# Kernel optimization log

Measured on AMD Instinct MI355X. Metric: run time of the kernel, lower is better.

## Reference

```python
import jax, jax.numpy as jnp
import numpy as np

N_HEAD = 8
EPS = 1e-6  # LayerNorm2d eps


def setup_inputs() -> dict:
    key = jax.random.key(0)
    ks = jax.random.split(key, 7)
    B, C, H, W = 16, 256, 128, 128
    nh, dk, dv = N_HEAD, 32, 32
    s = 1.0 / np.sqrt(C)
    return {
        "q": jax.random.normal(ks[0], (B, C, H, W), jnp.float32),
        "k": jax.random.normal(ks[1], (B, C, H, W), jnp.float32),
        "v": jax.random.normal(ks[2], (B, C, H, W), jnp.float32),
        # 1x1 convs without bias == channel matmuls; weight shape [out_ch, in_ch]
        "wq": jax.random.normal(ks[3], (nh * dk, C), jnp.float32) * s,
        "wk": jax.random.normal(ks[4], (nh * dk, C), jnp.float32) * s,
        "wv": jax.random.normal(ks[5], (nh * dv, C), jnp.float32) * s,
        "wfc": jax.random.normal(ks[6], (C, nh * dv), jnp.float32) * (1.0 / np.sqrt(nh * dv)),
        "ln_w": jnp.ones((C,), jnp.float32),
        "ln_b": jnp.zeros((C,), jnp.float32),
        "kernel": 5,
        "pad": 2,
    }


def _forward(q, k, v, wq, wk, wv, wfc, ln_w, ln_b, kernel, pad):
    B, C, H, W = q.shape
    nh = N_HEAD
    dk = wq.shape[0] // nh
    dv = wv.shape[0] // nh
    assert kernel == 2 * pad + 1
    residual = q
    # 1x1 conv projections, split into heads: [B, nh, d, H, W]
    qh = jnp.einsum('oc,bchw->bohw', wq, q).reshape(B, nh, dk, H, W)
    kh = jnp.einsum('oc,bchw->bohw', wk, k).reshape(B, nh, dk, H, W)
    vh = jnp.einsum('oc,bchw->bohw', wv, v).reshape(B, nh, dv, H, W)
    # zero-pad spatially: out-of-bounds correlations/values are zero, matching the
    # original bilinear sampler (zeros padding) and the custom padding() helper.
    kp = jnp.pad(kh, ((0, 0), (0, 0), (0, 0), (pad, pad), (pad, pad)))
    vp = jnp.pad(vh, ((0, 0), (0, 0), (0, 0), (pad, pad), (pad, pad)))
    # local correlation volume: dot(q[i,j], k[i+dy-pad, j+dx-pad]) for the KxK window
    # (integer offsets -> bilinear sample degenerates to a gather). Never materializes
    # the full [B, HW, HW] matrix the torch code builds before sampling.
    corr = jnp.stack(
        [jnp.einsum('bncij,bncij->bnij', qh, kp[:, :, :, dy:dy + H, dx:dx + W])
         for dy in range(kernel) for dx in range(kernel)], axis=-1)  # [B,nh,H,W,K*K]
    # relu (from CorrBlock.corr), temperature = sqrt(d_k), softmax over window.
    # OOB entries are 0 (not -inf), faithfully matching the original.
    attn = jax.nn.softmax(jax.nn.relu(corr) / jnp.float32(np.sqrt(dk)), axis=-1)
    # channel attention: per-pixel weighted sum of v over the same window
    out = jnp.zeros((B, nh, dv, H, W), q.dtype)
    idx = 0
    for dy in range(kernel):
        for dx in range(kernel):
            out = out + attn[:, :, :, :, idx][:, :, None] * vp[:, :, :, dy:dy + H, dx:dx + W]
            idx += 1
    o = jnp.einsum('oc,bchw->bohw', wfc, out.reshape(B, nh * dv, H, W)) + residual
    # LayerNorm2d: normalize over channel dim per pixel
    mu = o.mean(1, keepdims=True)
    var = ((o - mu) ** 2).mean(1, keepdims=True)
    y = (o - mu) / jnp.sqrt(var + EPS)
    return ln_w[None, :, None, None] * y + ln_b[None, :, None, None]


def reference(q, k, v, wq, wk, wv, wfc, ln_w, ln_b, kernel, pad):
    return _forward(q, k, v, wq, wk, wv, wfc, ln_w, ln_b, kernel, pad)
```

## Files before the change

kernel.cpp:

```cpp
#include <hip/hip_runtime.h>
#include <hip/hip_bf16.h>

#define BATCH 16
#define CH 256
#define HH 128
#define WW 128
#define HWSZ (HH * WW)
#define NHEAD 8
#define DHEAD 32
#define PW 132
#define PPIX (132 * 132)
#define ROWS 264

typedef __attribute__((ext_vector_type(8))) short bf16x8;
typedef __attribute__((ext_vector_type(4))) float f32x4;
typedef _Float16 h2v __attribute__((ext_vector_type(2)));

__device__ __forceinline__ unsigned short f2h(float f) {
    _Float16 h = (_Float16)f;
    return __builtin_bit_cast(unsigned short, h);
}
__device__ __forceinline__ unsigned pkbf(float a, float b) {
    __hip_bfloat162_raw r = __hip_bfloat162_raw(__float22bfloat162_rn(make_float2(a, b)));
    return (unsigned)r.x | ((unsigned)r.y << 16);
}

#if __has_builtin(__builtin_amdgcn_fdot2)
#define DOT2(a, b, c) __builtin_amdgcn_fdot2((a), (b), (c), false)
#else
#define DOT2(a, b, c) ((c) + (float)(a)[0] * (float)(b)[0] + (float)(a)[1] * (float)(b)[1])
#endif

__global__ __launch_bounds__(256)
void zpad_kernel(unsigned short* __restrict__ kpad, unsigned short* __restrict__ vpad)
{
    int bid = blockIdx.x;
    unsigned short* dst = ((bid & 1) ? vpad : kpad) + (size_t)(bid >> 1) * PPIX * DHEAD;
    const uint4 z = {0u, 0u, 0u, 0u};
    for (int i = threadIdx.x; i < 1040; i += 256) {
        int row, col;
        if (i < 264)      { row = i / 132; col = i - row * 132; }
        else if (i < 528) { int j = i - 264; int r = j / 132; row = 130 + r; col = j - r * 132; }
        else              { int j = i - 528; row = 2 + (j >> 2); int c = j & 3; col = (c < 2) ? c : (128 + c); }
        uint4* p = reinterpret_cast<uint4*>(dst + (size_t)(row * PW + col) * DHEAD);
        p[0] = z; p[1] = z; p[2] = z; p[3] = z;
    }
}

__global__ __launch_bounds__(256)
void prep_kernel(const float* __restrict__ wq, const float* __restrict__ wk,
                 const float* __restrict__ wv, const float* __restrict__ wfc,
                 unsigned short* __restrict__ wb)
{
    const float* src = (blockIdx.y == 0) ? wq : (blockIdx.y == 1) ? wk
                     : (blockIdx.y == 2) ? wv : wfc;
    unsigned short* dst = wb + blockIdx.y * 65536;
    int e = (blockIdx.x * 256 + threadIdx.x) * 8;
    const float4* s = reinterpret_cast<const float4*>(src + e);
    float4 a = s[0], c = s[1];
    uint4 u;
    u.x = pkbf(a.x, a.y); u.y = pkbf(a.z, a.w);
    u.z = pkbf(c.x, c.y); u.w = pkbf(c.z, c.w);
    *reinterpret_cast<uint4*>(dst + e) = u;
}

__global__ __launch_bounds__(512)
void proj_kernel(const float* __restrict__ q, const float* __restrict__ k,
                 const float* __restrict__ v, const unsigned short* __restrict__ wb,
                 unsigned short* __restrict__ qh, unsigned short* __restrict__ kpad,
                 unsigned short* __restrict__ vpad)
{
    __shared__ __align__(16) unsigned short lB[64 * ROWS];

    const int t = threadIdx.x;
    const int b = blockIdx.y;
    const int p0 = blockIdx.x * 64;
    const int z = blockIdx.z;

    const float* X; unsigned short* Y;
    if (z == 0)      { X = q; Y = qh; }
    else if (z == 1) { X = k; Y = kpad; }
    else             { X = v; Y = vpad; }
    const unsigned short* Wb = wb + z * 65536;
    X += (size_t)b * CH * HWSZ;
    const size_t pixstride = (z == 0) ? (size_t)HWSZ : (size_t)PPIX;
    Y += (size_t)b * NHEAD * pixstride * DHEAD;

    const int lane = t & 63;
    const int wid  = t >> 6;
    const int lrow = lane & 15;
    const int lkg  = lane >> 4;
    const int pB   = t & 63;
    const int cg   = t >> 6;
    const int psw  = pB >> 3;

    float fv[32];
    {
        const float* xb = X + p0 + pB + (size_t)(cg * 32) * HWSZ;
#pragma unroll
        for (int i = 0; i < 32; ++i) fv[i] = xb[(size_t)i * HWSZ];
    }
    __builtin_amdgcn_sched_barrier(0);
#pragma unroll
    for (int i = 0; i < 4; ++i) {
        uint4 u;
        u.x = pkbf(fv[i*8+0], fv[i*8+1]); u.y = pkbf(fv[i*8+2], fv[i*8+3]);
        u.z = pkbf(fv[i*8+4], fv[i*8+5]); u.w = pkbf(fv[i*8+6], fv[i*8+7]);
        *reinterpret_cast<uint4*>(&lB[pB * ROWS + ((cg * 4 + i) ^ psw) * 8]) = u;
    }

    bf16x8 afc[2], afn[2];
#pragma unroll
    for (int m = 0; m < 2; ++m)
        afc[m] = *reinterpret_cast<const bf16x8*>(Wb + (wid * 32 + m * 16 + lrow) * 256 + lkg * 8);

    f32x4 acc[2][4];
    const f32x4 zero = {0.f, 0.f, 0.f, 0.f};
#pragma unroll
    for (int m = 0; m < 2; ++m)
#pragma unroll
        for (int n = 0; n < 4; ++n) acc[m][n] = zero;

    __syncthreads();

#pragma unroll
    for (int ks = 0; ks < 8; ++ks) {
        if (ks < 7) {
#pragma unroll
            for (int m = 0; m < 2; ++m)
                afn[m] = *reinterpret_cast<const bf16x8*>(Wb + (wid * 32 + m * 16 + lrow) * 256 + (ks + 1) * 32 + lkg * 8);
        }
        bf16x8 bfv[4];
#pragma unroll
        for (int n = 0; n < 4; ++n) {
            int row = n * 16 + lrow;
            bfv[n] = *reinterpret_cast<const bf16x8*>(&lB[row * ROWS + ((ks * 4 + lkg) ^ (row >> 3)) * 8]);
        }
#pragma unroll
        for (int m = 0; m < 2; ++m)
#pragma unroll
            for (int n = 0; n < 4; ++n)
                acc[m][n] = __builtin_amdgcn_mfma_f32_16x16x32_bf16(afc[m], bfv[n], acc[m][n], 0, 0, 0);
#pragma unroll
        for (int m = 0; m < 2; ++m) afc[m] = afn[m];
    }

    const int lr = lane >> 4, lc = lane & 15;
#pragma unroll
    for (int m = 0; m < 2; ++m)
#pragma unroll
        for (int n = 0; n < 4; ++n) {
            int d0 = m * 16 + lr * 4;
            int p = p0 + n * 16 + lc;
            ushort4 pk;
            pk.x = f2h(acc[m][n][0]); pk.y = f2h(acc[m][n][1]);
            pk.z = f2h(acc[m][n][2]); pk.w = f2h(acc[m][n][3]);
            size_t pix;
            if (z == 0) pix = (size_t)wid * HWSZ + p;
            else { int row = p >> 7, col = p & 127; pix = (size_t)wid * PPIX + (size_t)(row + 2) * PW + (col + 2); }
            *reinterpret_cast<ushort4*>(&Y[pix * DHEAD + d0]) = pk;
        }
}

__global__ __launch_bounds__(1024)
void attn_kernel(unsigned short* __restrict__ qh,
                 const unsigned short* __restrict__ kpad,
                 const unsigned short* __restrict__ vpad)
{
    const int t = threadIdx.x;
    const int swz = (blockIdx.x & 7) * 1024 + (blockIdx.x >> 3);
    const int bh = swz >> 6;
    const int tile = swz & 63;
    const int x0 = (tile & 7) * 16, y0 = (tile >> 3) * 16;
    const int qc = t & 3;
    const int px = (t >> 2) & 15;
    const int py = t >> 6;
    const int gx = x0 + px, gy = y0 + py;

    unsigned short* qp = qh + ((size_t)bh * HWSZ + gy * WW + gx) * DHEAD + qc * 8;
    const unsigned short* kb = kpad + (size_t)bh * PPIX * DHEAD + qc * 8;
    const unsigned short* vb = vpad + (size_t)bh * PPIX * DHEAD + qc * 8;

    union { uint4 u; h2v h2[4]; } Q;
    Q.u = *reinterpret_cast<const uint4*>(qp);

    float ew[25];
#pragma unroll
    for (int wy = 0; wy < 5; ++wy) {
        const unsigned short* krow = kb + (size_t)((gy + wy) * PW + gx) * DHEAD;
#pragma unroll
        for (int wx = 0; wx < 5; ++wx) {
            union { uint4 u; h2v h2[4]; } K;
            K.u = *reinterpret_cast<const uint4*>(krow + wx * DHEAD);
            float s = 0.f;
#pragma unroll
            for (int j = 0; j < 4; ++j)
                s = DOT2(Q.h2[j], K.h2[j], s);
            s += __shfl_xor(s, 1);
            s += __shfl_xor(s, 2);
            ew[wy * 5 + wx] = __expf(fmaxf(s, 0.f) * 0.17677669529663687f);
        }
    }

    float sum = 0.f;
#pragma unroll
    for (int i = 0; i < 25; ++i) sum += ew[i];
    const float inv = 1.f / sum;

    union { uint4 u; h2v h2[4]; } A;
    const h2v hz = {(_Float16)0.f, (_Float16)0.f};
#pragma unroll
    for (int j = 0; j < 4; ++j) A.h2[j] = hz;

#pragma unroll
    for (int wy = 0; wy < 5; ++wy) {
        const unsigned short* vrow = vb + (size_t)((gy + wy) * PW + gx) * DHEAD;
#pragma unroll
        for (int wx = 0; wx < 5; ++wx) {
            _Float16 wh = (_Float16)(ew[wy * 5 + wx] * inv);
            h2v w2 = {wh, wh};
            union { uint4 u; h2v h2[4]; } V;
            V.u = *reinterpret_cast<const uint4*>(vrow + wx * DHEAD);
#pragma unroll
            for (int j = 0; j < 4; ++j)
                A.h2[j] += w2 * V.h2[j];
        }
    }

    uint4 o;
    o.x = pkbf((float)A.h2[0][0], (float)A.h2[0][1]);
    o.y = pkbf((float)A.h2[1][0], (float)A.h2[1][1]);
    o.z = pkbf((float)A.h2[2][0], (float)A.h2[2][1]);
    o.w = pkbf((float)A.h2[3][0], (float)A.h2[3][1]);
    *reinterpret_cast<uint4*>(qp) = o;
}

__global__ __launch_bounds__(512)
void fcln_kernel(const unsigned short* __restrict__ ob, const unsigned short* __restrict__ wfcb,
                 const float* __restrict__ qres, const float* __restrict__ lnw,
                 const float* __restrict__ lnb, float* __restrict__ out)
{
    __shared__ __align__(16) unsigned short lB[64 * ROWS];
    __shared__ float lsum[8][64];
    __shared__ float lssq[8][64];

    const int t = threadIdx.x;
    const int b = blockIdx.y;
    const int p0 = blockIdx.x * 64;

    const int lane = t & 63;
    const int wid  = t >> 6;
    const int lrow = lane & 15;
    const int lkg  = lane >> 4;

    uint4 bv[4];
#pragma unroll
    for (int r = 0; r < 4; ++r) {
        int idx = r * 512 + t;
        int h  = idx >> 8;
        int rem = idx & 255;
        int px = rem >> 2, qc = rem & 3;
        bv[r] = *reinterpret_cast<const uint4*>(
            ob + ((size_t)(b * NHEAD + h) * HWSZ + p0 + px) * DHEAD + qc * 8);
    }
    __builtin_amdgcn_sched_barrier(0);
#pragma unroll
    for (int r = 0; r < 4; ++r) {
        int idx = r * 512 + t;
        int h  = idx >> 8;
        int rem = idx & 255;
        int px = rem >> 2, qc = rem & 3;
        *reinterpret_cast<uint4*>(&lB[px * ROWS + ((h * 4 + qc) ^ (px >> 3)) * 8]) = bv[r];
    }

    bf16x8 afc[2], afn[2];
#pragma unroll
    for (int m = 0; m < 2; ++m)
        afc[m] = *reinterpret_cast<const bf16x8*>(wfcb + (wid * 32 + m * 16 + lrow) * 256 + lkg * 8);

    f32x4 acc[2][4];
    const f32x4 zero = {0.f, 0.f, 0.f, 0.f};
#pragma unroll
    for (int m = 0; m < 2; ++m)
#pragma unroll
        for (int n = 0; n < 4; ++n) acc[m][n] = zero;

    __syncthreads();

#pragma unroll
    for (int ks = 0; ks < 8; ++ks) {
        if (ks < 7) {
#pragma unroll
            for (int m = 0; m < 2; ++m)
                afn[m] = *reinterpret_cast<const bf16x8*>(wfcb + (wid * 32 + m * 16 + lrow) * 256 + (ks + 1) * 32 + lkg * 8);
        }
        bf16x8 bfv[4];
#pragma unroll
        for (int n = 0; n < 4; ++n) {
            int row = n * 16 + lrow;
            bfv[n] = *reinterpret_cast<const bf16x8*>(&lB[row * ROWS + ((ks * 4 + lkg) ^ (row >> 3)) * 8]);
        }
#pragma unroll
        for (int m = 0; m < 2; ++m)
#pragma unroll
            for (int n = 0; n < 4; ++n)
                acc[m][n] = __builtin_amdgcn_mfma_f32_16x16x32_bf16(afc[m], bfv[n], acc[m][n], 0, 0, 0);
#pragma unroll
        for (int m = 0; m < 2; ++m) afc[m] = afn[m];
    }

    const int lr = lane >> 4, lc = lane & 15;
    const float* qb = qres + (size_t)b * CH * HWSZ;
#pragma unroll
    for (int m = 0; m < 2; ++m)
#pragma unroll
        for (int n = 0; n < 4; ++n)
#pragma unroll
            for (int j = 0; j < 4; ++j) {
                int o = wid * 32 + m * 16 + lr * 4 + j;
                int p = p0 + n * 16 + lc;
                acc[m][n][j] += qb[(size_t)o * HWSZ + p];
            }

    float s[4], s2[4];
#pragma unroll
    for (int n = 0; n < 4; ++n) {
        float a = 0.f, c2 = 0.f;
#pragma unroll
        for (int m = 0; m < 2; ++m)
#pragma unroll
            for (int j = 0; j < 4; ++j) {
                float x = acc[m][n][j];
                a += x; c2 += x * x;
            }
        a  += __shfl_xor(a, 16);  a  += __shfl_xor(a, 32);
        c2 += __shfl_xor(c2, 16); c2 += __shfl_xor(c2, 32);
        s[n] = a; s2[n] = c2;
    }
    if (lane < 16) {
#pragma unroll
        for (int n = 0; n < 4; ++n) {
            lsum[wid][n * 16 + lane] = s[n];
            lssq[wid][n * 16 + lane] = s2[n];
        }
    }
    __syncthreads();

    float mu[4], rs[4];
#pragma unroll
    for (int n = 0; n < 4; ++n) {
        int p = n * 16 + lc;
        float ts = 0.f, tq = 0.f;
#pragma unroll
        for (int w = 0; w < 8; ++w) { ts += lsum[w][p]; tq += lssq[w][p]; }
        float m_ = ts * (1.f / 256.f);
        float v_ = tq * (1.f / 256.f) - m_ * m_;
        mu[n] = m_;
        rs[n] = rsqrtf(v_ + 1e-6f);
    }

    float* op = out + (size_t)b * CH * HWSZ;
#pragma unroll
    for (int m = 0; m < 2; ++m)
#pragma unroll
        for (int j = 0; j < 4; ++j) {
            int o = wid * 32 + m * 16 + lr * 4 + j;
            float g = lnw[o], bb = lnb[o];
#pragma unroll
            for (int n = 0; n < 4; ++n) {
                int p = p0 + n * 16 + lc;
                op[(size_t)o * HWSZ + p] = (acc[m][n][j] - mu[n]) * rs[n] * g + bb;
            }
        }
}

extern "C" void kernel_launch(void* const* d_in, const int* in_sizes, int n_in,
                              void* d_out, int out_size, void* d_ws, size_t ws_size,
                              hipStream_t stream) {
    const float* q   = (const float*)d_in[0];
    const float* k   = (const float*)d_in[1];
    const float* v   = (const float*)d_in[2];
    const float* wq  = (const float*)d_in[3];
    const float* wk  = (const float*)d_in[4];
    const float* wv  = (const float*)d_in[5];
    const float* wfc = (const float*)d_in[6];
    const float* lnw = (const float*)d_in[7];
    const float* lnb = (const float*)d_in[8];

    const size_t qsz = (size_t)BATCH * NHEAD * HWSZ * DHEAD;
    const size_t psz = (size_t)BATCH * NHEAD * PPIX * DHEAD;
    if (ws_size < (qsz + 2 * psz + 4 * 65536) * sizeof(unsigned short)) return;

    unsigned short* qh = (unsigned short*)d_ws;
    unsigned short* kp = qh + qsz;
    unsigned short* vp = kp + psz;
    unsigned short* wb = vp + psz;

    zpad_kernel<<<256, 256, 0, stream>>>(kp, vp);
    prep_kernel<<<dim3(32, 4), 256, 0, stream>>>(wq, wk, wv, wfc, wb);
    proj_kernel<<<dim3(HWSZ / 64, BATCH, 3), 512, 0, stream>>>(q, k, v, wb, qh, kp, vp);
    attn_kernel<<<8192, 1024, 0, stream>>>(qh, kp, vp);
    fcln_kernel<<<dim3(HWSZ / 64, BATCH), 512, 0, stream>>>(qh, wb + 3 * 65536, q, lnw, lnb, (float*)d_out);
}
```

Baseline: 783.7 us.

## Make projection and fc+LN kernels persistent with double-buffered LDS prefetch

The projection and fc+layernorm kernels now launch a fixed grid of 512 persistent blocks, each looping over several 64-pixel tiles (24 for projection, 8 for fc). The next tile's global loads are issued before the current tile's MFMA work and packed into a second LDS buffer afterward, overlapping memory latency with compute. The aim is to cut block launch overhead and hide load latency. In exchange, fv registers stay live across the loop, LDS use doubles, and parallelism is bounded by 512 blocks.

```diff
diff --git a/kernel.cpp b/kernel.cpp
--- a/kernel.cpp
+++ b/kernel.cpp
@@ -11,6 +11,9 @@
 #define PW 132
 #define PPIX (132 * 132)
 #define ROWS 264
+#define NBLK 512
+#define NITP 24
+#define NITF 8
 
 typedef __attribute__((ext_vector_type(8))) short bf16x8;
 typedef __attribute__((ext_vector_type(4))) float f32x4;
@@ -64,28 +67,15 @@
     *reinterpret_cast<uint4*>(dst + e) = u;
 }
 
-__global__ __launch_bounds__(512)
+__global__ __launch_bounds__(512, 4)
 void proj_kernel(const float* __restrict__ q, const float* __restrict__ k,
                  const float* __restrict__ v, const unsigned short* __restrict__ wb,
                  unsigned short* __restrict__ qh, unsigned short* __restrict__ kpad,
                  unsigned short* __restrict__ vpad)
 {
-    __shared__ __align__(16) unsigned short lB[64 * ROWS];
+    __shared__ __align__(16) unsigned short lB[2][64 * ROWS];
 
     const int t = threadIdx.x;
-    const int b = blockIdx.y;
-    const int p0 = blockIdx.x * 64;
-    const int z = blockIdx.z;
-
-    const float* X; unsigned short* Y;
-    if (z == 0)      { X = q; Y = qh; }
-    else if (z == 1) { X = k; Y = kpad; }
-    else             { X = v; Y = vpad; }
-    const unsigned short* Wb = wb + z * 65536;
-    X += (size_t)b * CH * HWSZ;
-    const size_t pixstride = (z == 0) ? (size_t)HWSZ : (size_t)PPIX;
-    Y += (size_t)b * NHEAD * pixstride * DHEAD;
-
     const int lane = t & 63;
     const int wid  = t >> 6;
     const int lrow = lane & 15;
@@ -94,72 +84,103 @@
     const int cg   = t >> 6;
     const int psw  = pB >> 3;
 
+    const int gbase = blockIdx.x * NITP;
+
+    auto xptr = [&](int g) -> const float* {
+        int z = g >> 12, b = (g >> 8) & 15;
+        const float* X = (z == 0) ? q : (z == 1) ? k : v;
+        return X + (size_t)b * CH * HWSZ + (g & 255) * 64;
+    };
+
     float fv[32];
     {
-        const float* xb = X + p0 + pB + (size_t)(cg * 32) * HWSZ;
+        const float* xb = xptr(gbase) + pB + (size_t)(cg * 32) * HWSZ;
 #pragma unroll
         for (int i = 0; i < 32; ++i) fv[i] = xb[(size_t)i * HWSZ];
     }
-    __builtin_amdgcn_sched_barrier(0);
 #pragma unroll
     for (int i = 0; i < 4; ++i) {
         uint4 u;
         u.x = pkbf(fv[i*8+0], fv[i*8+1]); u.y = pkbf(fv[i*8+2], fv[i*8+3]);
         u.z = pkbf(fv[i*8+4], fv[i*8+5]); u.w = pkbf(fv[i*8+6], fv[i*8+7]);
-        *reinterpret_cast<uint4*>(&lB[pB * ROWS + ((cg * 4 + i) ^ psw) * 8]) = u;
-    }
-
-    bf16x8 afc[2], afn[2];
-#pragma unroll
-    for (int m = 0; m < 2; ++m)
-        afc[m] = *reinterpret_cast<const bf16x8*>(Wb + (wid * 32 + m * 16 + lrow) * 256 + lkg * 8);
-
-    f32x4 acc[2][4];
-    const f32x4 zero = {0.f, 0.f, 0.f, 0.f};
-#pragma unroll
-    for (int m = 0; m < 2; ++m)
-#pragma unroll
-        for (int n = 0; n < 4; ++n) acc[m][n] = zero;
-
+        *reinterpret_cast<uint4*>(&lB[0][pB * ROWS + ((cg * 4 + i) ^ psw) * 8]) = u;
+    }
     __syncthreads();
 
-#pragma unroll
-    for (int ks = 0; ks < 8; ++ks) {
-        if (ks < 7) {
-#pragma unroll
-            for (int m = 0; m < 2; ++m)
-                afn[m] = *reinterpret_cast<const bf16x8*>(Wb + (wid * 32 + m * 16 + lrow) * 256 + (ks + 1) * 32 + lkg * 8);
-        }
-        bf16x8 bfv[4];
-#pragma unroll
-        for (int n = 0; n < 4; ++n) {
-            int row = n * 16 + lrow;
-            bfv[n] = *reinterpret_cast<const bf16x8*>(&lB[row * ROWS + ((ks * 4 + lkg) ^ (row >> 3)) * 8]);
-        }
+    for (int it = 0; it < NITP; ++it) {
+        const int g = gbase + it;
+        const int z = g >> 12;
+        const int b = (g >> 8) & 15;
+        const int p0 = (g & 255) * 64;
+
+        if (it + 1 < NITP) {
+            const float* xb = xptr(g + 1) + pB + (size_t)(cg * 32) * HWSZ;
+#pragma unroll
+            for (int i = 0; i < 32; ++i) fv[i] = xb[(size_t)i * HWSZ];
+        }
+
+        const unsigned short* Wb = wb + z * 65536;
+        f32x4 acc[2][4];
+        const f32x4 zero = {0.f, 0.f, 0.f, 0.f};
 #pragma unroll
         for (int m = 0; m < 2; ++m)
 #pragma unroll
-            for (int n = 0; n < 4; ++n)
-                acc[m][n] = __builtin_amdgcn_mfma_f32_16x16x32_bf16(afc[m], bfv[n], acc[m][n], 0, 0, 0);
-#pragma unroll
-        for (int m = 0; m < 2; ++m) afc[m] = afn[m];
-    }
-
-    const int lr = lane >> 4, lc = lane & 15;
-#pragma unroll
-    for (int m = 0; m < 2; ++m)
-#pragma unroll
-        for (int n = 0; n < 4; ++n) {
-            int d0 = m * 16 + lr * 4;
-            int p = p0 + n * 16 + lc;
-            ushort4 pk;
-            pk.x = f2h(acc[m][n][0]); pk.y = f2h(acc[m][n][1]);
-            pk.z = f2h(acc[m][n][2]); pk.w = f2h(acc[m][n][3]);
-            size_t pix;
-            if (z == 0) pix = (size_t)wid * HWSZ + p;
-            else { int row = p >> 7, col = p & 127; pix = (size_t)wid * PPIX + (size_t)(row + 2) * PW + (col + 2); }
-            *reinterpret_cast<ushort4*>(&Y[pix * DHEAD + d0]) = pk;
-        }
+            for (int n = 0; n < 4; ++n) acc[m][n] = zero;
+
+#pragma unroll
+        for (int ks = 0; ks < 8; ++ks) {
+            bf16x8 af[2];
+#pragma unroll
+            for (int m = 0; m < 2; ++m)
+                af[m] = *reinterpret_cast<const bf16x8*>(Wb + (wid * 32 + m * 16 + lrow) * 256 + ks * 32 + lkg * 8);
+            bf16x8 bfv[4];
+#pragma unroll
+            for (int n = 0; n < 4; ++n) {
+                int row = n * 16 + lrow;
+                bfv[n] = *reinterpret_cast<const bf16x8*>(&lB[it & 1][row * ROWS + ((ks * 4 + lkg) ^ (row >> 3)) * 8]);
+            }
+#pragma unroll
+            for (int m = 0; m < 2; ++m)
+#pragma unroll
+                for (int n = 0; n < 4; ++n)
+                    acc[m][n] = __builtin_amdgcn_mfma_f32_16x16x32_bf16(af[m], bfv[n], acc[m][n], 0, 0, 0);
+        }
+
+        {
+            unsigned short* Y;
+            size_t pixstride;
+            if (z == 0)      { Y = qh;   pixstride = HWSZ; }
+            else if (z == 1) { Y = kpad; pixstride = PPIX; }
+            else             { Y = vpad; pixstride = PPIX; }
+            Y += (size_t)b * NHEAD * pixstride * DHEAD;
+            const int lr = lane >> 4, lc = lane & 15;
+#pragma unroll
+            for (int m = 0; m < 2; ++m)
+#pragma unroll
+                for (int n = 0; n < 4; ++n) {
+                    int d0 = m * 16 + lr * 4;
+                    int p = p0 + n * 16 + lc;
+                    ushort4 pk;
+                    pk.x = f2h(acc[m][n][0]); pk.y = f2h(acc[m][n][1]);
+                    pk.z = f2h(acc[m][n][2]); pk.w = f2h(acc[m][n][3]);
+                    size_t pix;
+                    if (z == 0) pix = (size_t)wid * HWSZ + p;
+                    else { int row = p >> 7, col = p & 127; pix = (size_t)wid * PPIX + (size_t)(row + 2) * PW + (col + 2); }
+                    *reinterpret_cast<ushort4*>(&Y[pix * DHEAD + d0]) = pk;
+                }
+        }
+
+        if (it + 1 < NITP) {
+#pragma unroll
+            for (int i = 0; i < 4; ++i) {
+                uint4 u;
+                u.x = pkbf(fv[i*8+0], fv[i*8+1]); u.y = pkbf(fv[i*8+2], fv[i*8+3]);
+                u.z = pkbf(fv[i*8+4], fv[i*8+5]); u.w = pkbf(fv[i*8+6], fv[i*8+7]);
+                *reinterpret_cast<uint4*>(&lB[(it + 1) & 1][pB * ROWS + ((cg * 4 + i) ^ psw) * 8]) = u;
+            }
+        }
+        __syncthreads();
+    }
 }
 
 __global__ __launch_bounds__(1024)
@@ -235,143 +256,152 @@
     *reinterpret_cast<uint4*>(qp) = o;
 }
 
-__global__ __launch_bounds__(512)
+__global__ __launch_bounds__(512, 4)
 void fcln_kernel(const unsigned short* __restrict__ ob, const unsigned short* __restrict__ wfcb,
                  const float* __restrict__ qres, const float* __restrict__ lnw,
                  const float* __restrict__ lnb, float* __restrict__ out)
 {
-    __shared__ __align__(16) unsigned short lB[64 * ROWS];
+    __shared__ __align__(16) unsigned short lB[2][64 * ROWS];
     __shared__ float lsum[8][64];
     __shared__ float lssq[8][64];
 
     const int t = threadIdx.x;
-    const int b = blockIdx.y;
-    const int p0 = blockIdx.x * 64;
-
     const int lane = t & 63;
     const int wid  = t >> 6;
     const int lrow = lane & 15;
     const int lkg  = lane >> 4;
 
+    const int gbase = blockIdx.x * NITF;
+
+    auto stage_load = [&](int g, uint4* bv) {
+        const int b = g >> 8;
+        const int p0 = (g & 255) * 64;
+#pragma unroll
+        for (int r = 0; r < 4; ++r) {
+            int idx = r * 512 + t;
+            int h = idx >> 8;
+            int rem = idx & 255;
+            int px = rem >> 2, qc = rem & 3;
+            bv[r] = *reinterpret_cast<const uint4*>(
+                ob + ((size_t)(b * NHEAD + h) * HWSZ + p0 + px) * DHEAD + qc * 8);
+        }
+    };
+    auto stage_pack = [&](int buf, const uint4* bv) {
+#pragma unroll
+        for (int r = 0; r < 4; ++r) {
+            int idx = r * 512 + t;
+            int h = idx >> 8;
+            int rem = idx & 255;
+            int px = rem >> 2, qc = rem & 3;
+            *reinterpret_cast<uint4*>(&lB[buf][px * ROWS + ((h * 4 + qc) ^ (px >> 3)) * 8]) = bv[r];
+        }
+    };
+
     uint4 bv[4];
-#pragma unroll
-    for (int r = 0; r < 4; ++r) {
-        int idx = r * 512 + t;
-        int h  = idx >> 8;
-        int rem = idx & 255;
-        int px = rem >> 2, qc = rem & 3;
-        bv[r] = *reinterpret_cast<const uint4*>(
-            ob + ((size_t)(b * NHEAD + h) * HWSZ + p0 + px) * DHEAD + qc * 8);
-    }
-    __builtin_amdgcn_sched_barrier(0);
-#pragma unroll
-    for (int r = 0; r < 4; ++r) {
-        int idx = r * 512 + t;
-        int h  = idx >> 8;
-        int rem = idx & 255;
-        int px = rem >> 2, qc = rem & 3;
-        *reinterpret_cast<uint4*>(&lB[px * ROWS + ((h * 4 + qc) ^ (px >> 3)) * 8]) = bv[r];
-    }
-
-    bf16x8 afc[2], afn[2];
-#pragma unroll
-    for (int m = 0; m < 2; ++m)
-        afc[m] = *reinterpret_cast<const bf16x8*>(wfcb + (wid * 32 + m * 16 + lrow) * 256 + lkg * 8);
-
-    f32x4 acc[2][4];
-    const f32x4 zero = {0.f, 0.f, 0.f, 0.f};
-#pragma unroll
-    for (int m = 0; m < 2; ++m)
-#pragma unroll
-        for (int n = 0; n < 4; ++n) acc[m][n] = zero;
-
+    stage_load(gbase, bv);
+    stage_pack(0, bv);
     __syncthreads();
 
-#pragma unroll
-    for (int ks = 0; ks < 8; ++ks) {
-        if (ks < 7) {
-#pragma unroll
-            for (int m = 0; m < 2; ++m)
-                afn[m] = *reinterpret_cast<const bf16x8*>(wfcb + (wid * 32 + m * 16 + lrow) * 256 + (ks + 1) * 32 + lkg * 8);
-        }
-        bf16x8 bfv[4];
+    for (int it = 0; it < NITF; ++it) {
+        const int g = gbase + it;
+        const int b = g >> 8;
+        const int p0 = (g & 255) * 64;
+
+        if (it + 1 < NITF) stage_load(g + 1, bv);
+
+        f32x4 acc[2][4];
+        const f32x4 zero = {0.f, 0.f, 0.f, 0.f};
+#pragma unroll
+        for (int m = 0; m < 2; ++m)
+#pragma unroll
+            for (int n = 0; n < 4; ++n) acc[m][n] = zero;
+
+#pragma unroll
+        for (int ks = 0; ks < 8; ++ks) {
+            bf16x8 af[2];
+#pragma unroll
+            for (int m = 0; m < 2; ++m)
+                af[m] = *reinterpret_cast<const bf16x8*>(wfcb + (wid * 32 + m * 16 + lrow) * 256 + ks * 32 + lkg * 8);
+            bf16x8 bfv[4];
+#pragma unroll
+            for (int n = 0; n < 4; ++n) {
+                int row = n * 16 + lrow;
+                bfv[n] = *reinterpret_cast<const bf16x8*>(&lB[it & 1][row * ROWS + ((ks * 4 + lkg) ^ (row >> 3)) * 8]);
+            }
+#pragma unroll
+            for (int m = 0; m < 2; ++m)
+#pragma unroll
+                for (int n = 0; n < 4; ++n)
+                    acc[m][n] = __builtin_amdgcn_mfma_f32_16x16x32_bf16(af[m], bfv[n], acc[m][n], 0, 0, 0);
+        }
+
+        const int lr = lane >> 4, lc = lane & 15;
+        const float* qb = qres + (size_t)b * CH * HWSZ;
+#pragma unroll
+        for (int m = 0; m < 2; ++m)
+#pragma unroll
+            for (int n = 0; n < 4; ++n)
+#pragma unroll
+                for (int j = 0; j < 4; ++j) {
+                    int o = wid * 32 + m * 16 + lr * 4 + j;
+                    int p = p0 + n * 16 + lc;
+                    acc[m][n][j] += qb[(size_t)o * HWSZ + p];
+                }
+
+        float s[4], s2[4];
 #pragma unroll
         for (int n = 0; n < 4; ++n) {
-            int row = n * 16 + lrow;
-            bfv[n] = *reinterpret_cast<const bf16x8*>(&lB[row * ROWS + ((ks * 4 + lkg) ^ (row >> 3)) * 8]);
-        }
+            float a = 0.f, c2 = 0.f;
+#pragma unroll
+            for (int m = 0; m < 2; ++m)
+#pragma unroll
+                for (int j = 0; j < 4; ++j) {
+                    float x = acc[m][n][j];
+                    a += x; c2 += x * x;
+                }
+            a  += __shfl_xor(a, 16);  a  += __shfl_xor(a, 32);
+            c2 += __shfl_xor(c2, 16); c2 += __shfl_xor(c2, 32);
+            s[n] = a; s2[n] = c2;
+        }
+        if (lane < 16) {
+#pragma unroll
+            for (int n = 0; n < 4; ++n) {
+                lsum[wid][n * 16 + lane] = s[n];
+                lssq[wid][n * 16 + lane] = s2[n];
+            }
+        }
+        __syncthreads();
+
+        float mu[4], rs[4];
+#pragma unroll
+        for (int n = 0; n < 4; ++n) {
+            int p = n * 16 + lc;
+            float ts = 0.f, tq = 0.f;
+#pragma unroll
+            for (int w = 0; w < 8; ++w) { ts += lsum[w][p]; tq += lssq[w][p]; }
+            float m_ = ts * (1.f / 256.f);
+            float v_ = tq * (1.f / 256.f) - m_ * m_;
+            mu[n] = m_;
+            rs[n] = rsqrtf(v_ + 1e-6f);
+        }
+
+        float* op = out + (size_t)b * CH * HWSZ;
 #pragma unroll
         for (int m = 0; m < 2; ++m)
-#pragma unroll
-            for (int n = 0; n < 4; ++n)
-                acc[m][n] = __builtin_amdgcn_mfma_f32_16x16x32_bf16(afc[m], bfv[n], acc[m][n], 0, 0, 0);
-#pragma unroll
-        for (int m = 0; m < 2; ++m) afc[m] = afn[m];
-    }
-
-    const int lr = lane >> 4, lc = lane & 15;
-    const float* qb = qres + (size_t)b * CH * HWSZ;
-#pragma unroll
-    for (int m = 0; m < 2; ++m)
-#pragma unroll
-        for (int n = 0; n < 4; ++n)
 #pragma unroll
             for (int j = 0; j < 4; ++j) {
                 int o = wid * 32 + m * 16 + lr * 4 + j;
-                int p = p0 + n * 16 + lc;
-                acc[m][n][j] += qb[(size_t)o * HWSZ + p];
+                float g_ = lnw[o], bb = lnb[o];
+#pragma unroll
+                for (int n = 0; n < 4; ++n) {
+                    int p = p0 + n * 16 + lc;
+                    op[(size_t)o * HWSZ + p] = (acc[m][n][j] - mu[n]) * rs[n] * g_ + bb;
+                }
             }
 
-    float s[4], s2[4];
-#pragma unroll
-    for (int n = 0; n < 4; ++n) {
-        float a = 0.f, c2 = 0.f;
-#pragma unroll
-        for (int m = 0; m < 2; ++m)
-#pragma unroll
-            for (int j = 0; j < 4; ++j) {
-                float x = acc[m][n][j];
-                a += x; c2 += x * x;
-            }
-        a  += __shfl_xor(a, 16);  a  += __shfl_xor(a, 32);
-        c2 += __shfl_xor(c2, 16); c2 += __shfl_xor(c2, 32);
-        s[n] = a; s2[n] = c2;
-    }
-    if (lane < 16) {
-#pragma unroll
-        for (int n = 0; n < 4; ++n) {
-            lsum[wid][n * 16 + lane] = s[n];
-            lssq[wid][n * 16 + lane] = s2[n];
-        }
-    }
-    __syncthreads();
-
-    float mu[4], rs[4];
-#pragma unroll
-    for (int n = 0; n < 4; ++n) {
-        int p = n * 16 + lc;
-        float ts = 0.f, tq = 0.f;
-#pragma unroll
-        for (int w = 0; w < 8; ++w) { ts += lsum[w][p]; tq += lssq[w][p]; }
-        float m_ = ts * (1.f / 256.f);
-        float v_ = tq * (1.f / 256.f) - m_ * m_;
-        mu[n] = m_;
-        rs[n] = rsqrtf(v_ + 1e-6f);
-    }
-
-    float* op = out + (size_t)b * CH * HWSZ;
-#pragma unroll
-    for (int m = 0; m < 2; ++m)
-#pragma unroll
-        for (int j = 0; j < 4; ++j) {
-            int o = wid * 32 + m * 16 + lr * 4 + j;
-            float g = lnw[o], bb = lnb[o];
-#pragma unroll
-            for (int n = 0; n < 4; ++n) {
-                int p = p0 + n * 16 + lc;
-                op[(size_t)o * HWSZ + p] = (acc[m][n][j] - mu[n]) * rs[n] * g + bb;
-            }
-        }
+        if (it + 1 < NITF) stage_pack((it + 1) & 1, bv);
+        __syncthreads();
+    }
 }
 
 extern "C" void kernel_launch(void* const* d_in, const int* in_sizes, int n_in,
@@ -398,7 +428,7 @@
 
     zpad_kernel<<<256, 256, 0, stream>>>(kp, vp);
     prep_kernel<<<dim3(32, 4), 256, 0, stream>>>(wq, wk, wv, wfc, wb);
-    proj_kernel<<<dim3(HWSZ / 64, BATCH, 3), 512, 0, stream>>>(q, k, v, wb, qh, kp, vp);
+    proj_kernel<<<NBLK, 512, 0, stream>>>(q, k, v, wb, qh, kp, vp);
     attn_kernel<<<8192, 1024, 0, stream>>>(qh, kp, vp);
-    fcln_kernel<<<dim3(HWSZ / 64, BATCH), 512, 0, stream>>>(qh, wb + 3 * 65536, q, lnw, lnb, (float*)d_out);
-}
+    fcln_kernel<<<NBLK, 512, 0, stream>>>(qh, wb + 3 * 65536, q, lnw, lnb, (float*)d_out);
+}
```

Measured after the change: 1.134 ms. 1.45x slower.

## Stage weight tiles through double-buffered LDS and vectorize input loads in GEMM kernels

Applied to the files above, without the earlier changes.

In the projection and fc+LayerNorm kernels, each wave used to read its A-operand weight fragments straight from global memory. Now all 512 threads cooperatively load each K-slice of the weight matrix into a double-buffered LDS tile with a padded stride. The projection kernel's activation load also changes from 32 scalar loads per thread to eight float4 loads, packed per pixel into LDS, and the XOR swizzle on the B tile is dropped. The change adds about 40KB of LDS per block and a barrier per K-step, which may lower occupancy and reintroduce LDS bank conflicts on B reads.

```diff
diff --git a/kernel.cpp b/kernel.cpp
--- a/kernel.cpp
+++ b/kernel.cpp
@@ -11,6 +11,7 @@
 #define PW 132
 #define PPIX (132 * 132)
 #define ROWS 264
+#define ASTR 40
 
 typedef __attribute__((ext_vector_type(8))) short bf16x8;
 typedef __attribute__((ext_vector_type(4))) float f32x4;
@@ -71,6 +72,7 @@
                  unsigned short* __restrict__ vpad)
 {
     __shared__ __align__(16) unsigned short lB[64 * ROWS];
+    __shared__ __align__(16) unsigned short lA[2][256 * ASTR];
 
     const int t = threadIdx.x;
     const int b = blockIdx.y;
@@ -90,29 +92,34 @@
     const int wid  = t >> 6;
     const int lrow = lane & 15;
     const int lkg  = lane >> 4;
-    const int pB   = t & 63;
-    const int cg   = t >> 6;
-    const int psw  = pB >> 3;
-
-    float fv[32];
+    const int pxq  = t & 15;
+    const int oct  = t >> 4;
+    const int ao0 = t >> 1,       ak0 = (t & 1) * 2;
+
     {
-        const float* xb = X + p0 + pB + (size_t)(cg * 32) * HWSZ;
-#pragma unroll
-        for (int i = 0; i < 32; ++i) fv[i] = xb[(size_t)i * HWSZ];
-    }
-    __builtin_amdgcn_sched_barrier(0);
-#pragma unroll
-    for (int i = 0; i < 4; ++i) {
+        const float* xb = X + p0 + pxq * 4 + (size_t)(oct * 8) * HWSZ;
+        float4 f0 = *reinterpret_cast<const float4*>(xb + 0 * HWSZ);
+        float4 f1 = *reinterpret_cast<const float4*>(xb + 1 * HWSZ);
+        float4 f2 = *reinterpret_cast<const float4*>(xb + 2 * HWSZ);
+        float4 f3 = *reinterpret_cast<const float4*>(xb + 3 * HWSZ);
+        float4 f4 = *reinterpret_cast<const float4*>(xb + 4 * HWSZ);
+        float4 f5 = *reinterpret_cast<const float4*>(xb + 5 * HWSZ);
+        float4 f6 = *reinterpret_cast<const float4*>(xb + 6 * HWSZ);
+        float4 f7 = *reinterpret_cast<const float4*>(xb + 7 * HWSZ);
         uint4 u;
-        u.x = pkbf(fv[i*8+0], fv[i*8+1]); u.y = pkbf(fv[i*8+2], fv[i*8+3]);
-        u.z = pkbf(fv[i*8+4], fv[i*8+5]); u.w = pkbf(fv[i*8+6], fv[i*8+7]);
-        *reinterpret_cast<uint4*>(&lB[pB * ROWS + ((cg * 4 + i) ^ psw) * 8]) = u;
-    }
-
-    bf16x8 afc[2], afn[2];
-#pragma unroll
-    for (int m = 0; m < 2; ++m)
-        afc[m] = *reinterpret_cast<const bf16x8*>(Wb + (wid * 32 + m * 16 + lrow) * 256 + lkg * 8);
+#define PACKJ(J, C) \
+        u.x = pkbf(f0.C, f1.C); u.y = pkbf(f2.C, f3.C); \
+        u.z = pkbf(f4.C, f5.C); u.w = pkbf(f6.C, f7.C); \
+        *reinterpret_cast<uint4*>(&lB[(pxq * 4 + J) * ROWS + oct * 8]) = u;
+        PACKJ(0, x) PACKJ(1, y) PACKJ(2, z) PACKJ(3, w)
+#undef PACKJ
+    }
+    {
+        uint4 w0 = *reinterpret_cast<const uint4*>(Wb + ao0 * 256 + ak0 * 8);
+        uint4 w1 = *reinterpret_cast<const uint4*>(Wb + ao0 * 256 + ak0 * 8 + 8);
+        *reinterpret_cast<uint4*>(&lA[0][ao0 * ASTR + ak0 * 8]) = w0;
+        *reinterpret_cast<uint4*>(&lA[0][ao0 * ASTR + ak0 * 8 + 8]) = w1;
+    }
 
     f32x4 acc[2][4];
     const f32x4 zero = {0.f, 0.f, 0.f, 0.f};
@@ -125,24 +132,28 @@
 
 #pragma unroll
     for (int ks = 0; ks < 8; ++ks) {
+        uint4 w0, w1;
         if (ks < 7) {
-#pragma unroll
-            for (int m = 0; m < 2; ++m)
-                afn[m] = *reinterpret_cast<const bf16x8*>(Wb + (wid * 32 + m * 16 + lrow) * 256 + (ks + 1) * 32 + lkg * 8);
-        }
-        bf16x8 bfv[4];
-#pragma unroll
-        for (int n = 0; n < 4; ++n) {
-            int row = n * 16 + lrow;
-            bfv[n] = *reinterpret_cast<const bf16x8*>(&lB[row * ROWS + ((ks * 4 + lkg) ^ (row >> 3)) * 8]);
-        }
+            w0 = *reinterpret_cast<const uint4*>(Wb + ao0 * 256 + (ks + 1) * 32 + ak0 * 8);
+            w1 = *reinterpret_cast<const uint4*>(Wb + ao0 * 256 + (ks + 1) * 32 + ak0 * 8 + 8);
+        }
+        bf16x8 af[2], bfv[4];
 #pragma unroll
         for (int m = 0; m < 2; ++m)
+            af[m] = *reinterpret_cast<const bf16x8*>(&lA[ks & 1][(wid * 32 + m * 16 + lrow) * ASTR + lkg * 8]);
+#pragma unroll
+        for (int n = 0; n < 4; ++n)
+            bfv[n] = *reinterpret_cast<const bf16x8*>(&lB[(n * 16 + lrow) * ROWS + (ks * 4 + lkg) * 8]);
+#pragma unroll
+        for (int m = 0; m < 2; ++m)
 #pragma unroll
             for (int n = 0; n < 4; ++n)
-                acc[m][n] = __builtin_amdgcn_mfma_f32_16x16x32_bf16(afc[m], bfv[n], acc[m][n], 0, 0, 0);
-#pragma unroll
-        for (int m = 0; m < 2; ++m) afc[m] = afn[m];
+                acc[m][n] = __builtin_amdgcn_mfma_f32_16x16x32_bf16(af[m], bfv[n], acc[m][n], 0, 0, 0);
+        if (ks < 7) {
+            *reinterpret_cast<uint4*>(&lA[(ks + 1) & 1][ao0 * ASTR + ak0 * 8]) = w0;
+            *reinterpret_cast<uint4*>(&lA[(ks + 1) & 1][ao0 * ASTR + ak0 * 8 + 8]) = w1;
+            __syncthreads();
+        }
     }
 
     const int lr = lane >> 4, lc = lane & 15;
@@ -241,6 +252,7 @@
                  const float* __restrict__ lnb, float* __restrict__ out)
 {
     __shared__ __align__(16) unsigned short lB[64 * ROWS];
+    __shared__ __align__(16) unsigned short lA[2][256 * ASTR];
     __shared__ float lsum[8][64];
     __shared__ float lssq[8][64];
 
@@ -252,31 +264,24 @@
     const int wid  = t >> 6;
     const int lrow = lane & 15;
     const int lkg  = lane >> 4;
-
-    uint4 bv[4];
+    const int ao0 = t >> 1, ak0 = (t & 1) * 2;
+
 #pragma unroll
     for (int r = 0; r < 4; ++r) {
         int idx = r * 512 + t;
-        int h  = idx >> 8;
+        int h = idx >> 8;
         int rem = idx & 255;
         int px = rem >> 2, qc = rem & 3;
-        bv[r] = *reinterpret_cast<const uint4*>(
+        uint4 bv = *reinterpret_cast<const uint4*>(
             ob + ((size_t)(b * NHEAD + h) * HWSZ + p0 + px) * DHEAD + qc * 8);
-    }
-    __builtin_amdgcn_sched_barrier(0);
-#pragma unroll
-    for (int r = 0; r < 4; ++r) {
-        int idx = r * 512 + t;
-        int h  = idx >> 8;
-        int rem = idx & 255;
-        int px = rem >> 2, qc = rem & 3;
-        *reinterpret_cast<uint4*>(&lB[px * ROWS + ((h * 4 + qc) ^ (px >> 3)) * 8]) = bv[r];
-    }
-
-    bf16x8 afc[2], afn[2];
-#pragma unroll
-    for (int m = 0; m < 2; ++m)
-        afc[m] = *reinterpret_cast<const bf16x8*>(wfcb + (wid * 32 + m * 16 + lrow) * 256 + lkg * 8);
+        *reinterpret_cast<uint4*>(&lB[px * ROWS + (h * 4 + qc) * 8]) = bv;
+    }
+    {
+        uint4 w0 = *reinterpret_cast<const uint4*>(wfcb + ao0 * 256 + ak0 * 8);
+        uint4 w1 = *reinterpret_cast<const uint4*>(wfcb + ao0 * 256 + ak0 * 8 + 8);
+        *reinterpret_cast<uint4*>(&lA[0][ao0 * ASTR + ak0 * 8]) = w0;
+        *reinterpret_cast<uint4*>(&lA[0][ao0 * ASTR + ak0 * 8 + 8]) = w1;
+    }
 
     f32x4 acc[2][4];
     const f32x4 zero = {0.f, 0.f, 0.f, 0.f};
@@ -289,24 +294,28 @@
 
 #pragma unroll
     for (int ks = 0; ks < 8; ++ks) {
+        uint4 w0, w1;
         if (ks < 7) {
-#pragma unroll
-            for (int m = 0; m < 2; ++m)
-                afn[m] = *reinterpret_cast<const bf16x8*>(wfcb + (wid * 32 + m * 16 + lrow) * 256 + (ks + 1) * 32 + lkg * 8);
-        }
-        bf16x8 bfv[4];
-#pragma unroll
-        for (int n = 0; n < 4; ++n) {
-            int row = n * 16 + lrow;
-            bfv[n] = *reinterpret_cast<const bf16x8*>(&lB[row * ROWS + ((ks * 4 + lkg) ^ (row >> 3)) * 8]);
-        }
+            w0 = *reinterpret_cast<const uint4*>(wfcb + ao0 * 256 + (ks + 1) * 32 + ak0 * 8);
+            w1 = *reinterpret_cast<const uint4*>(wfcb + ao0 * 256 + (ks + 1) * 32 + ak0 * 8 + 8);
+        }
+        bf16x8 af[2], bfv[4];
 #pragma unroll
         for (int m = 0; m < 2; ++m)
+            af[m] = *reinterpret_cast<const bf16x8*>(&lA[ks & 1][(wid * 32 + m * 16 + lrow) * ASTR + lkg * 8]);
+#pragma unroll
+        for (int n = 0; n < 4; ++n)
+            bfv[n] = *reinterpret_cast<const bf16x8*>(&lB[(n * 16 + lrow) * ROWS + (ks * 4 + lkg) * 8]);
+#pragma unroll
+        for (int m = 0; m < 2; ++m)
 #pragma unroll
             for (int n = 0; n < 4; ++n)
-                acc[m][n] = __builtin_amdgcn_mfma_f32_16x16x32_bf16(afc[m], bfv[n], acc[m][n], 0, 0, 0);
-#pragma unroll
-        for (int m = 0; m < 2; ++m) afc[m] = afn[m];
+                acc[m][n] = __builtin_amdgcn_mfma_f32_16x16x32_bf16(af[m], bfv[n], acc[m][n], 0, 0, 0);
+        if (ks < 7) {
+            *reinterpret_cast<uint4*>(&lA[(ks + 1) & 1][ao0 * ASTR + ak0 * 8]) = w0;
+            *reinterpret_cast<uint4*>(&lA[(ks + 1) & 1][ao0 * ASTR + ak0 * 8 + 8]) = w1;
+            __syncthreads();
+        }
     }
 
     const int lr = lane >> 4, lc = lane & 15;
@@ -337,6 +346,7 @@
         c2 += __shfl_xor(c2, 16); c2 += __shfl_xor(c2, 32);
         s[n] = a; s2[n] = c2;
     }
+    __syncthreads();
     if (lane < 16) {
 #pragma unroll
         for (int n = 0; n < 4; ++n) {
```

Result: faster. 725.0 us (-7.5%).
